# Optimization experiments

Measured on AMD Instinct MI355X. Metric: run time of the kernel, lower is better.

The kernel has to match this reference:

```python
import jax, jax.numpy as jnp
import numpy as np

S, B, C = 7, 2, 20
L_COORD, POS_CONF, POS_CLS, L_NOOBJ = 5.0, 1.0, 1.0, 0.5
IMG_SIZE, GRID_SIZE = 448.0, 64.0
EPS = 1e-6


def setup_inputs() -> dict:
    key = jax.random.key(0)
    k1, k2 = jax.random.split(key)
    N = 16384
    predictions = jax.random.uniform(k1, (N, S, S, B * 5 + C), dtype=jnp.float32)
    target = jax.random.uniform(k2, (N, S, S, 5 + C), dtype=jnp.float32)
    return {"predictions": predictions, "target": target}


def _iou(pred_boxes, gt_boxes, gx, gy):
    # pred_boxes: [N,S,S,B,4] (x,y offsets in cell, w,h rel. to image)
    # gt_boxes:   [N,S,S,1,4]
    # gx, gy:     broadcastable grid indices [1,S,S,1]
    def corners(b):
        cx = (gx + b[..., 0]) * GRID_SIZE   # absolute center x (pixels)
        cy = (gy + b[..., 1]) * GRID_SIZE
        w = b[..., 2] * IMG_SIZE
        h = b[..., 3] * IMG_SIZE
        return cx - w / 2, cy - h / 2, cx + w / 2, cy + h / 2, w * h

    px1, py1, px2, py2, pa = corners(pred_boxes)
    gx1, gy1, gx2, gy2, ga = corners(gt_boxes)
    iw = jnp.clip(jnp.minimum(px2, gx2) - jnp.maximum(px1, gx1), 0.0)
    ih = jnp.clip(jnp.minimum(py2, gy2) - jnp.maximum(py1, gy1), 0.0)
    inter = iw * ih
    union = pa + ga - inter
    return inter / (union + EPS)   # [N,S,S,B]


def reference(predictions, target):
    N = predictions.shape[0]
    pred_boxes = predictions[..., : B * 5].reshape(N, S, S, B, 5)
    pred_cls = predictions[..., B * 5:]          # [N,S,S,C]
    gt_box = target[..., :5][..., None, :]       # [N,S,S,1,5]
    gt_cls = target[..., 5:]                     # [N,S,S,C]

    obj = (target[..., 4] > 0.5).astype(predictions.dtype)  # [N,S,S]

    gx = jnp.arange(S, dtype=predictions.dtype)[None, None, :, None]  # col index
    gy = jnp.arange(S, dtype=predictions.dtype)[None, :, None, None]  # row index

    iou = _iou(pred_boxes[..., :4], gt_box[..., :4], gx, gy)  # [N,S,S,B]

    # responsible box: max-IoU predictor per obj cell
    resp = jax.nn.one_hot(jnp.argmax(iou, axis=-1), B, dtype=predictions.dtype)  # [N,S,S,B]
    resp_obj = resp * obj[..., None]

    # coordinate loss (x, y, sqrt(w), sqrt(h))
    dxy = jnp.sum((pred_boxes[..., :2] - gt_box[..., :2]) ** 2, axis=-1)
    dwh = jnp.sum((jnp.sqrt(jnp.clip(pred_boxes[..., 2:4], 0.0))
                   - jnp.sqrt(jnp.clip(gt_box[..., 2:4], 0.0))) ** 2, axis=-1)
    loss_coord = L_COORD * jnp.sum(resp_obj * (dxy + dwh))

    # confidence loss: responsible box targets its IoU; others target 0
    conf = pred_boxes[..., 4]
    iou_t = jax.lax.stop_gradient(iou)
    loss_conf_obj = POS_CONF * jnp.sum(resp_obj * (conf - iou_t) ** 2)
    loss_conf_noobj = L_NOOBJ * jnp.sum((1.0 - resp_obj) * conf ** 2)

    # class loss on obj cells
    loss_cls = POS_CLS * jnp.sum(obj * jnp.sum((pred_cls - gt_cls) ** 2, axis=-1))

    return (loss_coord + loss_conf_obj + loss_conf_noobj + loss_cls) / N
```

## Files before the change

### kernel.cpp

```cpp
#include <hip/hip_runtime.h>


#define S7 7
#define CELL_P 30
#define CELL_T 25
#define PADP 31
#define PADT 27

__global__ __launch_bounds__(256) void yolo_cell_kernel(
    const float* __restrict__ pred, const float* __restrict__ tgt,
    float* __restrict__ partial)
{
    __shared__ float sp[256 * PADP];
    __shared__ float st[256 * PADT];

    const int t = threadIdx.x;

    {
        const float2* p2 = reinterpret_cast<const float2*>(
            pred + (size_t)blockIdx.x * 256 * CELL_P);
        #pragma unroll
        for (int i = 0; i < 15; ++i) {
            int j2 = t + 256 * i;
            float2 v = p2[j2];
            int cell = j2 / 15;
            int off  = 2 * (j2 - cell * 15);
            sp[cell * PADP + off]     = v.x;
            sp[cell * PADP + off + 1] = v.y;
        }
    }
    {
        const float2* t2 = reinterpret_cast<const float2*>(
            tgt + (size_t)blockIdx.x * 256 * CELL_T);
        #pragma unroll
        for (int i = 0; i < 13; ++i) {
            int j2 = t + 256 * i;
            if (i < 12 || j2 < 3200) {
                float2 v = t2[j2];
                int w  = 2 * j2;
                int c0 = w / 25;
                int o0 = w - c0 * 25;
                st[c0 * PADT + o0] = v.x;
                int w1 = w + 1;
                int c1 = w1 / 25;
                int o1 = w1 - c1 * 25;
                st[c1 * PADT + o1] = v.y;
            }
        }
    }
    __syncthreads();

    const float* pv = sp + t * PADP;
    const float* tv = st + t * PADT;

    int cell = blockIdx.x * 256 + t;
    int rem  = cell % 49;
    float gx = (float)(rem % S7);
    float gy = (float)(rem / S7);

    float obj = (tv[4] > 0.5f) ? 1.0f : 0.0f;

    float gcx = (gx + tv[0]) * 64.0f;
    float gcy = (gy + tv[1]) * 64.0f;
    float gw  = tv[2] * 448.0f;
    float gh  = tv[3] * 448.0f;
    float gx1 = gcx - gw * 0.5f, gy1 = gcy - gh * 0.5f;
    float gx2 = gcx + gw * 0.5f, gy2 = gcy + gh * 0.5f;
    float ga  = gw * gh;

    float iou[2], dxy[2], dwh[2], conf[2];
    #pragma unroll
    for (int b = 0; b < 2; ++b) {
        float b0 = pv[b * 5 + 0], b1 = pv[b * 5 + 1], b2 = pv[b * 5 + 2];
        float b3 = pv[b * 5 + 3], b4 = pv[b * 5 + 4];
        float pcx = (gx + b0) * 64.0f;
        float pcy = (gy + b1) * 64.0f;
        float pw  = b2 * 448.0f;
        float ph  = b3 * 448.0f;
        float px1 = pcx - pw * 0.5f, py1 = pcy - ph * 0.5f;
        float px2 = pcx + pw * 0.5f, py2 = pcy + ph * 0.5f;
        float pa  = pw * ph;

        float iw = fmaxf(fminf(px2, gx2) - fmaxf(px1, gx1), 0.0f);
        float ih = fmaxf(fminf(py2, gy2) - fmaxf(py1, gy1), 0.0f);
        float inter = iw * ih;
        iou[b] = inter / (pa + ga - inter + 1e-6f);

        float dx = b0 - tv[0], dy = b1 - tv[1];
        dxy[b] = dx * dx + dy * dy;
        float sw = sqrtf(fmaxf(b2, 0.0f)) - sqrtf(fmaxf(tv[2], 0.0f));
        float sh = sqrtf(fmaxf(b3, 0.0f)) - sqrtf(fmaxf(tv[3], 0.0f));
        dwh[b] = sw * sw + sh * sh;
        conf[b] = b4;
    }

    int best = (iou[1] > iou[0]) ? 1 : 0;

    float loss = 0.0f;
    #pragma unroll
    for (int b = 0; b < 2; ++b) {
        float resp_obj = (b == best) ? obj : 0.0f;
        loss += 5.0f * resp_obj * (dxy[b] + dwh[b]);
        float d = conf[b] - iou[b];
        loss += resp_obj * d * d;
        loss += 0.5f * (1.0f - resp_obj) * conf[b] * conf[b];
    }

    float cls = 0.0f;
    #pragma unroll
    for (int c = 0; c < 20; ++c) {
        float d = pv[10 + c] - tv[5 + c];
        cls += d * d;
    }
    loss += obj * cls;

    #pragma unroll
    for (int off = 32; off > 0; off >>= 1)
        loss += __shfl_down(loss, off, 64);

    __shared__ float smem[4];
    int lane = t & 63;
    int wid  = t >> 6;
    if (lane == 0) smem[wid] = loss;
    __syncthreads();
    if (t == 0)
        partial[blockIdx.x] = smem[0] + smem[1] + smem[2] + smem[3];
}

__global__ __launch_bounds__(256) void yolo_final_kernel(
    const float* __restrict__ partial, int n, float* __restrict__ out, float invN)
{
    float s = 0.0f;
    for (int i = threadIdx.x; i < n; i += 256)
        s += partial[i];
    #pragma unroll
    for (int off = 32; off > 0; off >>= 1)
        s += __shfl_down(s, off, 64);

    __shared__ float smem[4];
    int lane = threadIdx.x & 63;
    int wid  = threadIdx.x >> 6;
    if (lane == 0) smem[wid] = s;
    __syncthreads();
    if (threadIdx.x == 0)
        out[0] = (smem[0] + smem[1] + smem[2] + smem[3]) * invN;
}

extern "C" void kernel_launch(void* const* d_in, const int* in_sizes, int n_in,
                              void* d_out, int out_size, void* d_ws, size_t ws_size,
                              hipStream_t stream)
{
    const float* pred = (const float*)d_in[0];
    const float* tgt  = (const float*)d_in[1];
    float* out        = (float*)d_out;
    float* partial    = (float*)d_ws;

    int ncells = in_sizes[0] / CELL_P;
    int N      = ncells / 49;
    int blocks = ncells / 256;

    yolo_cell_kernel<<<blocks, 256, 0, stream>>>(pred, tgt, partial);
    yolo_final_kernel<<<1, 256, 0, stream>>>(partial, blocks, out, 1.0f / (float)N);
}
```

Before: 40.94 us.

## Persistent fused loss kernel with register-prefetched tiles and last-block reduction

Replaces the one-tile-per-block kernel plus separate final reduction with 512 persistent blocks. Each block loops over its cells, prefetching the next tile into registers while computing on the current shared-memory tile. A last-block atomic counter performs the final reduction in the same kernel. It also stores tiles unpadded in shared memory, which may cause bank conflicts on the per-thread reads. It adds a memset launch and the counter synchronization.

```diff
diff --git a/kernel.cpp b/kernel.cpp
--- a/kernel.cpp
+++ b/kernel.cpp
@@ -4,56 +4,47 @@
 #define S7 7
 #define CELL_P 30
 #define CELL_T 25
-#define PADP 31
-#define PADT 27
-
-__global__ __launch_bounds__(256) void yolo_cell_kernel(
-    const float* __restrict__ pred, const float* __restrict__ tgt,
-    float* __restrict__ partial)
-{
-    __shared__ float sp[256 * PADP];
-    __shared__ float st[256 * PADT];
-
-    const int t = threadIdx.x;
-
-    {
-        const float2* p2 = reinterpret_cast<const float2*>(
-            pred + (size_t)blockIdx.x * 256 * CELL_P);
-        #pragma unroll
-        for (int i = 0; i < 15; ++i) {
-            int j2 = t + 256 * i;
-            float2 v = p2[j2];
-            int cell = j2 / 15;
-            int off  = 2 * (j2 - cell * 15);
-            sp[cell * PADP + off]     = v.x;
-            sp[cell * PADP + off + 1] = v.y;
-        }
-    }
-    {
-        const float2* t2 = reinterpret_cast<const float2*>(
-            tgt + (size_t)blockIdx.x * 256 * CELL_T);
-        #pragma unroll
-        for (int i = 0; i < 13; ++i) {
-            int j2 = t + 256 * i;
-            if (i < 12 || j2 < 3200) {
-                float2 v = t2[j2];
-                int w  = 2 * j2;
-                int c0 = w / 25;
-                int o0 = w - c0 * 25;
-                st[c0 * PADT + o0] = v.x;
-                int w1 = w + 1;
-                int c1 = w1 / 25;
-                int o1 = w1 - c1 * 25;
-                st[c1 * PADT + o1] = v.y;
-            }
-        }
-    }
-    __syncthreads();
-
-    const float* pv = sp + t * PADP;
-    const float* tv = st + t * PADT;
-
-    int cell = blockIdx.x * 256 + t;
+#define TPB 256
+#define NBLK 512
+
+__device__ __forceinline__ void load_tile(const float2* __restrict__ p2,
+                                          const float2* __restrict__ t2,
+                                          int base_p, int base_t,
+                                          int lim_p, int lim_t, int t,
+                                          float2* rp, float2* rt)
+{
+    #pragma unroll
+    for (int i = 0; i < 15; ++i) {
+        int idx = t + TPB * i;
+        if (idx < lim_p) rp[i] = p2[base_p + idx];
+    }
+    #pragma unroll
+    for (int i = 0; i < 13; ++i) {
+        int idx = t + TPB * i;
+        if (idx < lim_t) rt[i] = t2[base_t + idx];
+    }
+}
+
+__device__ __forceinline__ void store_tile(float2* sp2, float2* st2,
+                                           int lim_p, int lim_t, int t,
+                                           const float2* rp, const float2* rt)
+{
+    #pragma unroll
+    for (int i = 0; i < 15; ++i) {
+        int idx = t + TPB * i;
+        if (idx < lim_p) sp2[idx] = rp[i];
+    }
+    #pragma unroll
+    for (int i = 0; i < 13; ++i) {
+        int idx = t + TPB * i;
+        if (idx < lim_t) st2[idx] = rt[i];
+    }
+}
+
+__device__ __forceinline__ float cell_loss(const float* __restrict__ pv,
+                                           const float* __restrict__ tv,
+                                           int cell)
+{
     int rem  = cell % 49;
     float gx = (float)(rem % S7);
     float gy = (float)(rem / S7);
@@ -112,38 +103,94 @@
         float d = pv[10 + c] - tv[5 + c];
         cls += d * d;
     }
-    loss += obj * cls;
+    return loss + obj * cls;
+}
+
+__global__ __launch_bounds__(TPB) void yolo_fused_kernel(
+    const float* __restrict__ pred, const float* __restrict__ tgt,
+    float* __restrict__ partial, unsigned int* __restrict__ cnt,
+    float* __restrict__ out, int cpb, float invN)
+{
+    __shared__ float sp[TPB * CELL_P];
+    __shared__ float st[TPB * CELL_T];
+    __shared__ float sred[4];
+    __shared__ bool  sdone;
+
+    const int t   = threadIdx.x;
+    const int bid = blockIdx.x;
+    if (t == 0) sdone = false;
+
+    const long long cell0 = (long long)bid * cpb;
+    const int fullTiles = cpb >> 8;
+    const int rem       = cpb & 255;
+    const int tiles     = fullTiles + (rem ? 1 : 0);
+
+    const float2* p2 = reinterpret_cast<const float2*>(pred + cell0 * CELL_P);
+    const float2* t2 = reinterpret_cast<const float2*>(tgt  + cell0 * CELL_T);
+    float2* sp2 = reinterpret_cast<float2*>(sp);
+    float2* st2 = reinterpret_cast<float2*>(st);
+
+    float2 rp[15], rt[13];
+    float  acc = 0.0f;
+
+    {
+        int lp = (0 < fullTiles) ? TPB * 15 : rem * 15;
+        int lt = (0 < fullTiles) ? (TPB * 25) / 2 : (rem * 25) / 2;
+        load_tile(p2, t2, 0, 0, lp, lt, t, rp, rt);
+    }
+
+    for (int f = 0; f < tiles; ++f) {
+        const bool full = (f < fullTiles);
+        const int  nc   = full ? TPB : rem;
+        const int  lp   = nc * 15;
+        const int  lt   = (nc * 25) >> 1;
+
+        __syncthreads();
+        store_tile(sp2, st2, lp, lt, t, rp, rt);
+
+        if (f + 1 < tiles) {
+            const bool nfull = (f + 1 < fullTiles);
+            const int  nnc   = nfull ? TPB : rem;
+            load_tile(p2, t2, (f + 1) * TPB * 15, (f + 1) * (TPB * 25 / 2),
+                      nnc * 15, (nnc * 25) >> 1, t, rp, rt);
+        }
+        __syncthreads();
+
+        if (t < nc)
+            acc += cell_loss(sp + t * CELL_P, st + t * CELL_T,
+                             (int)(cell0 + f * TPB + t));
+    }
 
     #pragma unroll
     for (int off = 32; off > 0; off >>= 1)
-        loss += __shfl_down(loss, off, 64);
-
-    __shared__ float smem[4];
+        acc += __shfl_down(acc, off, 64);
+
     int lane = t & 63;
     int wid  = t >> 6;
-    if (lane == 0) smem[wid] = loss;
+    if (lane == 0) sred[wid] = acc;
     __syncthreads();
-    if (t == 0)
-        partial[blockIdx.x] = smem[0] + smem[1] + smem[2] + smem[3];
-}
-
-__global__ __launch_bounds__(256) void yolo_final_kernel(
-    const float* __restrict__ partial, int n, float* __restrict__ out, float invN)
-{
-    float s = 0.0f;
-    for (int i = threadIdx.x; i < n; i += 256)
-        s += partial[i];
-    #pragma unroll
-    for (int off = 32; off > 0; off >>= 1)
-        s += __shfl_down(s, off, 64);
-
-    __shared__ float smem[4];
-    int lane = threadIdx.x & 63;
-    int wid  = threadIdx.x >> 6;
-    if (lane == 0) smem[wid] = s;
+    if (t == 0) {
+        partial[bid] = sred[0] + sred[1] + sred[2] + sred[3];
+        __threadfence();
+        unsigned int old = atomicAdd(cnt, 1u);
+        sdone = (old == (unsigned int)(gridDim.x - 1));
+    }
     __syncthreads();
-    if (threadIdx.x == 0)
-        out[0] = (smem[0] + smem[1] + smem[2] + smem[3]) * invN;
+
+    if (sdone) {
+        __threadfence();
+        float s = 0.0f;
+        for (int i = t; i < (int)gridDim.x; i += TPB)
+            s += partial[i];
+        #pragma unroll
+        for (int off = 32; off > 0; off >>= 1)
+            s += __shfl_down(s, off, 64);
+        __syncthreads();
+        if (lane == 0) sred[wid] = s;
+        __syncthreads();
+        if (t == 0)
+            out[0] = (sred[0] + sred[1] + sred[2] + sred[3]) * invN;
+    }
 }
 
 extern "C" void kernel_launch(void* const* d_in, const int* in_sizes, int n_in,
@@ -154,11 +201,13 @@
     const float* tgt  = (const float*)d_in[1];
     float* out        = (float*)d_out;
     float* partial    = (float*)d_ws;
+    unsigned int* cnt = (unsigned int*)((char*)d_ws + NBLK * sizeof(float));
 
     int ncells = in_sizes[0] / CELL_P;
     int N      = ncells / 49;
-    int blocks = ncells / 256;
-
-    yolo_cell_kernel<<<blocks, 256, 0, stream>>>(pred, tgt, partial);
-    yolo_final_kernel<<<1, 256, 0, stream>>>(partial, blocks, out, 1.0f / (float)N);
-}
+    int cpb    = ncells / NBLK;
+
+    hipMemsetAsync(cnt, 0, sizeof(unsigned int), stream);
+    yolo_fused_kernel<<<NBLK, TPB, 0, stream>>>(pred, tgt, partial, cnt, out,
+                                                cpb, 1.0f / (float)N);
+}
```

Measured after the change: 47.81 us. 1.17x slower.

## Use direct global-to-LDS loads with smaller blocks and split work across waves

Applied to the files above, without the earlier changes.

Replaces per-thread float2 loads and scattered LDS stores with 16-byte global_load_lds transfers into unpadded shared buffers. Blocks are shrunk to 64 cells with 128 threads: one wave computes box/IoU/confidence terms and the other computes the class loss. The final reduction uses 1024 threads to sum the larger number of partials. The aim is to cut the load/store instruction overhead and raise memory-level parallelism. The risks are LDS bank conflicts from the unpadded strides and more block scheduling overhead.

```diff
diff --git a/kernel.cpp b/kernel.cpp
--- a/kernel.cpp
+++ b/kernel.cpp
@@ -4,146 +4,147 @@
 #define S7 7
 #define CELL_P 30
 #define CELL_T 25
-#define PADP 31
-#define PADT 27
+#define TPB 128
+#define CPB 64
 
-__global__ __launch_bounds__(256) void yolo_cell_kernel(
+__device__ __forceinline__ void gload16(const void* g, void* l)
+{
+    __builtin_amdgcn_global_load_lds(
+        (const __attribute__((address_space(1))) unsigned int*)g,
+        (__attribute__((address_space(3))) unsigned int*)l, 16, 0, 0);
+}
+
+__global__ __launch_bounds__(TPB, 6) void yolo_cell_kernel(
     const float* __restrict__ pred, const float* __restrict__ tgt,
     float* __restrict__ partial)
 {
-    __shared__ float sp[256 * PADP];
-    __shared__ float st[256 * PADT];
+    __shared__ float sp[CPB * CELL_P];
+    __shared__ float st[CPB * CELL_T];
+    __shared__ float sred[2];
 
-    const int t = threadIdx.x;
+    const int t    = threadIdx.x;
+    const int lane = t & 63;
+    const int wid  = t >> 6;
+    const int bid  = blockIdx.x;
 
-    {
-        const float2* p2 = reinterpret_cast<const float2*>(
-            pred + (size_t)blockIdx.x * 256 * CELL_P);
+    const char* P = (const char*)(pred + (size_t)bid * CPB * CELL_P);
+    const char* T = (const char*)(tgt  + (size_t)bid * CPB * CELL_T);
+
+    if (wid == 0) {
         #pragma unroll
-        for (int i = 0; i < 15; ++i) {
-            int j2 = t + 256 * i;
-            float2 v = p2[j2];
-            int cell = j2 / 15;
-            int off  = 2 * (j2 - cell * 15);
-            sp[cell * PADP + off]     = v.x;
-            sp[cell * PADP + off + 1] = v.y;
-        }
-    }
-    {
-        const float2* t2 = reinterpret_cast<const float2*>(
-            tgt + (size_t)blockIdx.x * 256 * CELL_T);
+        for (int k = 0; k < 7; ++k)
+            gload16(P + k * 1024 + lane * 16, (char*)sp + k * 1024);
+    } else {
         #pragma unroll
-        for (int i = 0; i < 13; ++i) {
-            int j2 = t + 256 * i;
-            if (i < 12 || j2 < 3200) {
-                float2 v = t2[j2];
-                int w  = 2 * j2;
-                int c0 = w / 25;
-                int o0 = w - c0 * 25;
-                st[c0 * PADT + o0] = v.x;
-                int w1 = w + 1;
-                int c1 = w1 / 25;
-                int o1 = w1 - c1 * 25;
-                st[c1 * PADT + o1] = v.y;
-            }
-        }
+        for (int k = 0; k < 6; ++k)
+            gload16(T + k * 1024 + lane * 16, (char*)st + k * 1024);
+        if (lane < 32)
+            gload16(P + 7168 + lane * 16, (char*)sp + 7168);
+        if (lane < 16)
+            gload16(T + 6144 + lane * 16, (char*)st + 6144);
     }
     __syncthreads();
 
-    const float* pv = sp + t * PADP;
-    const float* tv = st + t * PADT;
+    float acc = 0.0f;
 
-    int cell = blockIdx.x * 256 + t;
-    int rem  = cell % 49;
-    float gx = (float)(rem % S7);
-    float gy = (float)(rem / S7);
+    if (wid == 0) {
+        const float* pv = sp + lane * CELL_P;
+        const float* tv = st + lane * CELL_T;
 
-    float obj = (tv[4] > 0.5f) ? 1.0f : 0.0f;
+        int cell = bid * CPB + lane;
+        int rem  = cell % 49;
+        float gx = (float)(rem % S7);
+        float gy = (float)(rem / S7);
 
-    float gcx = (gx + tv[0]) * 64.0f;
-    float gcy = (gy + tv[1]) * 64.0f;
-    float gw  = tv[2] * 448.0f;
-    float gh  = tv[3] * 448.0f;
-    float gx1 = gcx - gw * 0.5f, gy1 = gcy - gh * 0.5f;
-    float gx2 = gcx + gw * 0.5f, gy2 = gcy + gh * 0.5f;
-    float ga  = gw * gh;
+        float obj = (tv[4] > 0.5f) ? 1.0f : 0.0f;
 
-    float iou[2], dxy[2], dwh[2], conf[2];
-    #pragma unroll
-    for (int b = 0; b < 2; ++b) {
-        float b0 = pv[b * 5 + 0], b1 = pv[b * 5 + 1], b2 = pv[b * 5 + 2];
-        float b3 = pv[b * 5 + 3], b4 = pv[b * 5 + 4];
-        float pcx = (gx + b0) * 64.0f;
-        float pcy = (gy + b1) * 64.0f;
-        float pw  = b2 * 448.0f;
-        float ph  = b3 * 448.0f;
-        float px1 = pcx - pw * 0.5f, py1 = pcy - ph * 0.5f;
-        float px2 = pcx + pw * 0.5f, py2 = pcy + ph * 0.5f;
-        float pa  = pw * ph;
+        float gcx = (gx + tv[0]) * 64.0f;
+        float gcy = (gy + tv[1]) * 64.0f;
+        float gw  = tv[2] * 448.0f;
+        float gh  = tv[3] * 448.0f;
+        float gx1 = gcx - gw * 0.5f, gy1 = gcy - gh * 0.5f;
+        float gx2 = gcx + gw * 0.5f, gy2 = gcy + gh * 0.5f;
+        float ga  = gw * gh;
 
-        float iw = fmaxf(fminf(px2, gx2) - fmaxf(px1, gx1), 0.0f);
-        float ih = fmaxf(fminf(py2, gy2) - fmaxf(py1, gy1), 0.0f);
-        float inter = iw * ih;
-        iou[b] = inter / (pa + ga - inter + 1e-6f);
+        float iou[2], dxy[2], dwh[2], conf[2];
+        #pragma unroll
+        for (int b = 0; b < 2; ++b) {
+            float b0 = pv[b * 5 + 0], b1 = pv[b * 5 + 1], b2 = pv[b * 5 + 2];
+            float b3 = pv[b * 5 + 3], b4 = pv[b * 5 + 4];
+            float pcx = (gx + b0) * 64.0f;
+            float pcy = (gy + b1) * 64.0f;
+            float pw  = b2 * 448.0f;
+            float ph  = b3 * 448.0f;
+            float px1 = pcx - pw * 0.5f, py1 = pcy - ph * 0.5f;
+            float px2 = pcx + pw * 0.5f, py2 = pcy + ph * 0.5f;
+            float pa  = pw * ph;
 
-        float dx = b0 - tv[0], dy = b1 - tv[1];
-        dxy[b] = dx * dx + dy * dy;
-        float sw = sqrtf(fmaxf(b2, 0.0f)) - sqrtf(fmaxf(tv[2], 0.0f));
-        float sh = sqrtf(fmaxf(b3, 0.0f)) - sqrtf(fmaxf(tv[3], 0.0f));
-        dwh[b] = sw * sw + sh * sh;
-        conf[b] = b4;
+            float iw = fmaxf(fminf(px2, gx2) - fmaxf(px1, gx1), 0.0f);
+            float ih = fmaxf(fminf(py2, gy2) - fmaxf(py1, gy1), 0.0f);
+            float inter = iw * ih;
+            iou[b] = inter / (pa + ga - inter + 1e-6f);
+
+            float dx = b0 - tv[0], dy = b1 - tv[1];
+            dxy[b] = dx * dx + dy * dy;
+            float sw = sqrtf(fmaxf(b2, 0.0f)) - sqrtf(fmaxf(tv[2], 0.0f));
+            float sh = sqrtf(fmaxf(b3, 0.0f)) - sqrtf(fmaxf(tv[3], 0.0f));
+            dwh[b] = sw * sw + sh * sh;
+            conf[b] = b4;
+        }
+
+        int best = (iou[1] > iou[0]) ? 1 : 0;
+
+        #pragma unroll
+        for (int b = 0; b < 2; ++b) {
+            float resp_obj = (b == best) ? obj : 0.0f;
+            acc += 5.0f * resp_obj * (dxy[b] + dwh[b]);
+            float d = conf[b] - iou[b];
+            acc += resp_obj * d * d;
+            acc += 0.5f * (1.0f - resp_obj) * conf[b] * conf[b];
+        }
+    } else {
+        const float* pc = sp + lane * CELL_P + 10;
+        const float* tc = st + lane * CELL_T + 5;
+        float obj = (st[lane * CELL_T + 4] > 0.5f) ? 1.0f : 0.0f;
+
+        float cls = 0.0f;
+        #pragma unroll
+        for (int c = 0; c < 20; ++c) {
+            float d = pc[c] - tc[c];
+            cls += d * d;
+        }
+        acc = obj * cls;
     }
-
-    int best = (iou[1] > iou[0]) ? 1 : 0;
-
-    float loss = 0.0f;
-    #pragma unroll
-    for (int b = 0; b < 2; ++b) {
-        float resp_obj = (b == best) ? obj : 0.0f;
-        loss += 5.0f * resp_obj * (dxy[b] + dwh[b]);
-        float d = conf[b] - iou[b];
-        loss += resp_obj * d * d;
-        loss += 0.5f * (1.0f - resp_obj) * conf[b] * conf[b];
-    }
-
-    float cls = 0.0f;
-    #pragma unroll
-    for (int c = 0; c < 20; ++c) {
-        float d = pv[10 + c] - tv[5 + c];
-        cls += d * d;
-    }
-    loss += obj * cls;
 
     #pragma unroll
     for (int off = 32; off > 0; off >>= 1)
-        loss += __shfl_down(loss, off, 64);
-
-    __shared__ float smem[4];
-    int lane = t & 63;
-    int wid  = t >> 6;
-    if (lane == 0) smem[wid] = loss;
+        acc += __shfl_down(acc, off, 64);
+    if (lane == 0) sred[wid] = acc;
     __syncthreads();
-    if (t == 0)
-        partial[blockIdx.x] = smem[0] + smem[1] + smem[2] + smem[3];
+    if (t == 0) partial[bid] = sred[0] + sred[1];
 }
 
-__global__ __launch_bounds__(256) void yolo_final_kernel(
+__global__ __launch_bounds__(1024) void yolo_final_kernel(
     const float* __restrict__ partial, int n, float* __restrict__ out, float invN)
 {
     float s = 0.0f;
-    for (int i = threadIdx.x; i < n; i += 256)
+    for (int i = threadIdx.x; i < n; i += 1024)
         s += partial[i];
     #pragma unroll
     for (int off = 32; off > 0; off >>= 1)
         s += __shfl_down(s, off, 64);
 
-    __shared__ float smem[4];
+    __shared__ float smem[16];
     int lane = threadIdx.x & 63;
     int wid  = threadIdx.x >> 6;
     if (lane == 0) smem[wid] = s;
     __syncthreads();
-    if (threadIdx.x == 0)
-        out[0] = (smem[0] + smem[1] + smem[2] + smem[3]) * invN;
+    if (threadIdx.x == 0) {
+        float r = 0.0f;
+        #pragma unroll
+        for (int w = 0; w < 16; ++w) r += smem[w];
+        out[0] = r * invN;
+    }
 }
 
 extern "C" void kernel_launch(void* const* d_in, const int* in_sizes, int n_in,
@@ -157,8 +158,8 @@
 
     int ncells = in_sizes[0] / CELL_P;
     int N      = ncells / 49;
-    int blocks = ncells / 256;
+    int blocks = ncells / CPB;
 
-    yolo_cell_kernel<<<blocks, 256, 0, stream>>>(pred, tgt, partial);
-    yolo_final_kernel<<<1, 256, 0, stream>>>(partial, blocks, out, 1.0f / (float)N);
+    yolo_cell_kernel<<<blocks, TPB, 0, stream>>>(pred, tgt, partial);
+    yolo_final_kernel<<<1, 1024, 0, stream>>>(partial, blocks, out, 1.0f / (float)N);
 }
```

After: 35.27 us. 13.8% less time.
